# Optimization experiments

Measured on AMD Instinct MI355X. Metric: run time of the kernel, lower is better.

## Reference

```python
import jax, jax.numpy as jnp
import numpy as np

K_PRESERVED = 384   # num_preserved_tokens
NUM_HEADS = 6       # config.num_attention_heads // 2


def setup_inputs() -> dict:
    key = jax.random.key(0)
    ks = jax.random.split(key, 10)
    B, L, D, H = 16, 512, 768, 12
    U = D // 2  # num_units of the router attention
    s = 0.02
    return {
        "hidden_states": jax.random.normal(ks[0], (B, L, D), jnp.float32),
        "self_attention_scores": jax.random.uniform(ks[1], (B, H, L, L), jnp.float32),
        "Wq": jax.random.normal(ks[2], (D, U), jnp.float32) * s,
        "bq": jnp.zeros((U,), jnp.float32),
        "Wk": jax.random.normal(ks[3], (D, U), jnp.float32) * s,
        "bk": jnp.zeros((U,), jnp.float32),
        "Wv": jax.random.normal(ks[4], (D, U), jnp.float32) * s,
        "bv": jnp.zeros((U,), jnp.float32),
        "Wo": jax.random.normal(ks[5], (U, D), jnp.float32) * s,
        "bo": jnp.zeros((D,), jnp.float32),
    }


def _forward(hidden_states, self_attention_scores, Wq, bq, Wk, bk, Wv, bv, Wo, bo):
    B, L, D = hidden_states.shape
    K = K_PRESERVED
    r = L - K  # number of tokens merged away by ToMe
    batch_idx = jnp.arange(B)[:, None]

    class_token = hidden_states[:, :1, :]

    # importance = column sums of head-averaged attention with zeroed diagonal (detached)
    s = jax.lax.stop_gradient(jnp.mean(self_attention_scores, axis=1))  # [B,L,L]
    s = s * (1.0 - jnp.eye(L, dtype=s.dtype))
    importance = jnp.sum(s, axis=1)  # [B,L]
    _, important_idx = jax.lax.top_k(importance, K)  # [B,K]
    important_mask = jnp.zeros((B, L), bool).at[batch_idx, important_idx].set(True)

    # --- ToMe bipartite_soft_matching(hidden_states, r), mode='mean' ---
    metric = jax.lax.stop_gradient(hidden_states)
    metric = metric / jnp.linalg.norm(metric, axis=-1, keepdims=True)
    a, b = metric[:, ::2, :], metric[:, 1::2, :]            # [B,L/2,D] each
    sim = jnp.einsum('bid,bjd->bij', a, b)                   # [B,L/2,L/2]
    node_max = jnp.max(sim, axis=-1)                         # [B,L/2]
    node_idx = jnp.argmax(sim, axis=-1)                      # [B,L/2]
    edge_idx = jnp.argsort(-node_max, axis=-1)               # descending
    src_idx = edge_idx[:, :r]                                # merged src tokens
    unm_idx = edge_idx[:, r:]                                # unmerged src tokens
    dst_idx = jnp.take_along_axis(node_idx, src_idx, axis=1)  # [B,r]

    src_x = hidden_states[:, ::2, :]
    dst_x = hidden_states[:, 1::2, :]                        # [B,L/2,D]
    unm = jnp.take_along_axis(src_x, unm_idx[..., None], axis=1)   # [B,L/2-r,D]
    src_sel = jnp.take_along_axis(src_x, src_idx[..., None], axis=1)  # [B,r,D]
    # scatter_reduce(mean, include_self=True): (dst + sum srcs) / (1 + count)
    sums = dst_x.at[batch_idx, dst_idx].add(src_sel)
    counts = jnp.ones((B, L // 2), dst_x.dtype).at[batch_idx, dst_idx].add(1.0)
    dst_merged = sums / counts[..., None]
    preserved_tokens = jnp.concatenate([unm, dst_merged], axis=1)  # [B,K,D]

    # attention_mask is None -> sentences is the first token
    sentences = hidden_states[:, :1, :]

    # unpreserved tokens: boolean-mask gather, preserving original order
    order = jnp.argsort(important_mask.astype(jnp.int32), axis=1, stable=True)
    unp_idx = order[:, : L - K]                              # [B,L-K]
    unpreserved = hidden_states[batch_idx, unp_idx]          # [B,L-K,D]

    # router multi-head attention: query=sentence, key/value=unpreserved
    U = Wq.shape[1]
    hd = U // NUM_HEADS
    q = (sentences @ Wq + bq).reshape(B, 1, NUM_HEADS, hd)
    k = (unpreserved @ Wk + bk).reshape(B, L - K, NUM_HEADS, hd)
    v = (unpreserved @ Wv + bv).reshape(B, L - K, NUM_HEADS, hd)
    att = jax.nn.softmax(jnp.einsum('bqhd,bkhd->bhqk', q, k) / jnp.sqrt(jnp.asarray(hd, q.dtype)), axis=-1)
    ctx = jnp.einsum('bhqk,bkhd->bqhd', att, v).reshape(B, 1, U)
    new_token = ctx @ Wo + bo                                # [B,1,D]

    final_token = jnp.concatenate([class_token, preserved_tokens, new_token], axis=1)  # [B,K+2,D]
    return final_token


def reference(hidden_states, self_attention_scores, Wq, bq, Wk, bk, Wv, bv, Wo, bo):
    return _forward(hidden_states, self_attention_scores, Wq, bq, Wk, bk, Wv, bv, Wo, bo)
```

## Files before the change

kernel.cpp:

```cpp
#include <hip/hip_runtime.h>

#define BB 16
#define LL 512
#define DD 768
#define NHEAD 12
#define HALF 256
#define KPRES 384
#define RCNT 128
#define UDIM 384
#define NH2 6
#define HD 64

__device__ float              g_colsum_part[BB * NHEAD * 4 * LL];
__device__ unsigned long long g_nodep_part[BB * HALF * 4];
__device__ int g_unm[BB * RCNT];
__device__ int g_srctok[BB * RCNT];
__device__ int g_srcdst[BB * RCNT];
__device__ int g_unp[BB * RCNT];
__device__ float g_q[BB * UDIM];
__device__ float g_w2[BB * NH2 * DD];
__device__ float g_qbk[BB * NH2];
__device__ float g_ctx[BB * UDIM];

__global__ void k_main(const float* __restrict__ sc, const float* __restrict__ hs,
                       const float* __restrict__ Wq, const float* __restrict__ bq) {
    __shared__ __align__(16) float As[64][20];
    __shared__ __align__(16) float BsT[16][68];
    __shared__ float nA[64], nB[64];
    __shared__ unsigned long long cand[64][16];
    __shared__ float red[256];
    __shared__ __align__(16) float4 smc[256];
    __shared__ float h0q[DD];
    int blk = blockIdx.x;
    int t = threadIdx.x;

    if (blk >= 1024) {
        int qb = blk - 1024;
        int b = qb / NH2, h = qb % NH2;
        const float* hb = hs + (size_t)b * LL * DD;
        for (int d = t; d < DD; d += 256) h0q[d] = hb[d];
        __syncthreads();
        int u = t & 63, part = t >> 6;
        float a = 0.f;
        for (int d = part * 192; d < part * 192 + 192; d++)
            a += h0q[d] * Wq[(size_t)d * UDIM + h * HD + u];
        red[t] = a;
        __syncthreads();
        if (t < HD)
            g_q[b * UDIM + h * HD + t] =
                bq[h * HD + t] + red[t] + red[t + 64] + red[t + 128] + red[t + 192];
        return;
    }

    if (blk >= 256) {
        int cb = blk - 256;
        int ic = cb & 3;
        int bh = cb >> 2;
        const float* base = sc + (size_t)bh * LL * LL;
        int i0 = ic * 128;
        int p = t >> 7;
        int s = t & 127;
        float4 acc = {0.f, 0.f, 0.f, 0.f};
#pragma unroll 8
        for (int i = 0; i < 64; i++) {
            float4 v = ((const float4*)(base + (size_t)(i0 + 2 * i + p) * LL))[s];
            acc.x += v.x; acc.y += v.y; acc.z += v.z; acc.w += v.w;
        }
#pragma unroll
        for (int c = 0; c < 4; c++) {
            int cj = 4 * s + c;
            if (cj >= i0 && cj < i0 + 128 && (cj & 1) == p) {
                float d = base[(size_t)cj * LL + cj];
                if (c == 0) acc.x -= d; else if (c == 1) acc.y -= d;
                else if (c == 2) acc.z -= d; else acc.w -= d;
            }
        }
        smc[t] = acc;
        __syncthreads();
        if (t < 128) {
            float4 e = smc[t], o = smc[t + 128];
            float4 r;
            r.x = e.x + o.x; r.y = e.y + o.y; r.z = e.z + o.z; r.w = e.w + o.w;
            ((float4*)(g_colsum_part + (size_t)cb * LL))[t] = r;
        }
        return;
    }

    int b = blk >> 4, it = (blk >> 2) & 3, jt = blk & 3;
    int i0 = it * 64, j0 = jt * 64;
    const float* hb = hs + (size_t)b * LL * DD;
    {
        int rl = t >> 1, hf = t & 1;
        int grow = (rl < 64) ? 2 * (i0 + rl) : 2 * (j0 + rl - 64) + 1;
        const float4* rp = (const float4*)(hb + (size_t)grow * DD) + hf * 96;
        float4 ac = {0.f, 0.f, 0.f, 0.f};
#pragma unroll 4
        for (int q = 0; q < 96; q++) {
            float4 v = rp[q];
            ac.x += v.x * v.x; ac.y += v.y * v.y; ac.z += v.z * v.z; ac.w += v.w * v.w;
        }
        red[t] = (ac.x + ac.y) + (ac.z + ac.w);
        __syncthreads();
        if (t < 128) {
            float nrm = sqrtf(red[2 * t] + red[2 * t + 1]);
            if (t < 64) nA[t] = nrm; else nB[t - 64] = nrm;
        }
        __syncthreads();
    }
    int ti = t >> 4, tj = t & 15;
    float acc[4][4];
#pragma unroll
    for (int a = 0; a < 4; a++)
#pragma unroll
        for (int c = 0; c < 4; c++) acc[a][c] = 0.f;
    int sr = t >> 2, sc4 = t & 3;
    const float* arow = hb + (size_t)(2 * (i0 + sr)) * DD;
    const float* brow = hb + (size_t)(2 * (j0 + sr) + 1) * DD;
    float inA = nA[sr], inB = nB[sr];
    float4 a4 = ((const float4*)arow)[sc4];
    float4 b4 = ((const float4*)brow)[sc4];
    a4.x /= inA; a4.y /= inA; a4.z /= inA; a4.w /= inA;
    b4.x /= inB; b4.y /= inB; b4.z /= inB; b4.w /= inB;
    for (int s = 0; s < 48; s++) {
        __syncthreads();
        *(float4*)&As[sr][4 * sc4] = a4;
        BsT[4 * sc4 + 0][sr] = b4.x;
        BsT[4 * sc4 + 1][sr] = b4.y;
        BsT[4 * sc4 + 2][sr] = b4.z;
        BsT[4 * sc4 + 3][sr] = b4.w;
        __syncthreads();
        if (s + 1 < 48) {
            int d0 = (s + 1) * 16;
            a4 = ((const float4*)(arow + d0))[sc4];
            b4 = ((const float4*)(brow + d0))[sc4];
            a4.x /= inA; a4.y /= inA; a4.z /= inA; a4.w /= inA;
            b4.x /= inB; b4.y /= inB; b4.z /= inB; b4.w /= inB;
        }
#pragma unroll
        for (int c4 = 0; c4 < 4; c4++) {
            float4 av[4], bk4[4];
#pragma unroll
            for (int a = 0; a < 4; a++) av[a] = *(const float4*)&As[ti * 4 + a][4 * c4];
#pragma unroll
            for (int k = 0; k < 4; k++) bk4[k] = *(const float4*)&BsT[4 * c4 + k][4 * tj];
#pragma unroll
            for (int k = 0; k < 4; k++) {
#pragma unroll
                for (int a = 0; a < 4; a++) {
                    float ak = ((const float*)&av[a])[k];
#pragma unroll
                    for (int c = 0; c < 4; c++)
                        acc[a][c] += ak * ((const float*)&bk4[k])[c];
                }
            }
        }
    }
#pragma unroll
    for (int a = 0; a < 4; a++) {
        unsigned long long bp = 0ULL;
#pragma unroll
        for (int c = 0; c < 4; c++) {
            int jg = j0 + tj * 4 + c;
            unsigned u = __float_as_uint(acc[a][c]);
            u = (u & 0x80000000u) ? ~u : (u | 0x80000000u);
            unsigned long long pk = ((unsigned long long)u << 32) | (unsigned long long)(255 - jg);
            if (pk > bp) bp = pk;
        }
        cand[ti * 4 + a][tj] = bp;
    }
    __syncthreads();
    if (t < 64) {
        unsigned long long m = cand[t][0];
#pragma unroll
        for (int c2 = 1; c2 < 16; c2++) { unsigned long long v = cand[t][c2]; if (v > m) m = v; }
        g_nodep_part[((size_t)b * HALF + i0 + t) * 4 + jt] = m;
    }
}

__global__ void k_seledge(const float* __restrict__ Wk, const float* __restrict__ bk) {
    int blk = blockIdx.x, t = threadIdx.x;
    __shared__ float v[LL];
    __shared__ int pos[LL];
    __shared__ float nm[HALF];
    __shared__ int   ni[HALF];
    __shared__ __align__(16) float qsl[HD];

    if (blk >= BB) {
        int wb = blk - BB;
        int b = wb / NH2, h = wb % NH2;
        if (t < HD) qsl[t] = g_q[b * UDIM + h * HD + t];
        __syncthreads();
        if (t < 384) {
#pragma unroll
            for (int rep = 0; rep < 2; rep++) {
                int d = t + rep * 384;
                const float4* wrow = (const float4*)(Wk + (size_t)d * UDIM + h * HD);
                const float4* q4 = (const float4*)qsl;
                float4 s4 = {0.f, 0.f, 0.f, 0.f};
#pragma unroll
                for (int u4 = 0; u4 < 16; u4++) {
                    float4 w = wrow[u4], q = q4[u4];
                    s4.x += q.x * w.x; s4.y += q.y * w.y; s4.z += q.z * w.z; s4.w += q.w * w.w;
                }
                g_w2[((size_t)b * NH2 + h) * DD + d] = (s4.x + s4.y) + (s4.z + s4.w);
            }
        }
        if (t == 0) {
            float a = 0.f;
            for (int u = 0; u < HD; u++) a += qsl[u] * bk[h * HD + u];
            g_qbk[b * NH2 + h] = a;
        }
        return;
    }

    int b = blk;
    float imp = 0.f;
    for (int p = 0; p < NHEAD * 4; p++)
        imp += g_colsum_part[((size_t)b * NHEAD * 4 + p) * LL + t];
    v[t] = imp;
    __syncthreads();
    int cnt = 0;
    for (int k = 0; k < LL; k++) {
        float vk = v[k];
        cnt += (vk > imp) || (vk == imp && k < t);
    }
    int notp = (cnt >= KPRES) ? 1 : 0;
    pos[t] = notp;
    __syncthreads();
    for (int s = 1; s < LL; s <<= 1) {
        int add = (t >= s) ? pos[t - s] : 0;
        __syncthreads();
        pos[t] += add;
        __syncthreads();
    }
    if (notp) g_unp[b * RCNT + pos[t] - 1] = t;
    if (t < HALF) {
        unsigned long long p = g_nodep_part[((size_t)b * HALF + t) * 4 + 0];
#pragma unroll
        for (int q = 1; q < 4; q++) {
            unsigned long long w = g_nodep_part[((size_t)b * HALF + t) * 4 + q];
            if (w > p) p = w;
        }
        unsigned u = (unsigned)(p >> 32);
        unsigned bits = (u & 0x80000000u) ? (u & 0x7FFFFFFFu) : ~u;
        nm[t] = __uint_as_float(bits);
        ni[t] = 255 - (int)(p & 0xFFFFFFFFu);
    }
    __syncthreads();
    if (t < HALF) {
        float vv = nm[t];
        int cnt2 = 0;
        for (int k = 0; k < HALF; k++) {
            float vk = nm[k];
            cnt2 += (vk > vv) || (vk == vv && k < t);
        }
        if (cnt2 < RCNT) {
            g_srctok[b * RCNT + cnt2] = t;
            g_srcdst[b * RCNT + cnt2] = ni[t];
        } else {
            g_unm[b * RCNT + (cnt2 - RCNT)] = 2 * t;
        }
    }
}

__global__ void k_attn(const float* __restrict__ hs,
                       const float* __restrict__ Wv, const float* __restrict__ bv,
                       float* __restrict__ out) {
    int blk = blockIdx.x;
    int t = threadIdx.x;
    __shared__ __align__(16) float w2s[DD];
    __shared__ __align__(16) float hbars[DD];
    __shared__ int   toks[RCNT];
    __shared__ float att[RCNT];
    __shared__ float red[256];
    __shared__ float pm[4];
    __shared__ float qbkS;
    __shared__ int ss[RCNT], sd[RCNT];

    if (blk < BB * NH2) {
        int b = blk / NH2, h = blk % NH2;
        const float* hb = hs + (size_t)b * LL * DD;
        if (t < RCNT) toks[t] = g_unp[b * RCNT + t];
        for (int d = t; d < DD; d += 256) w2s[d] = g_w2[((size_t)b * NH2 + h) * DD + d];
        if (t == 0) qbkS = g_qbk[b * NH2 + h];
        __syncthreads();
        {
            int tok = t >> 1, half = t & 1;
            const float4* hr4 = (const float4*)(hb + (size_t)toks[tok] * DD) + half * 96;
            const float4* wk4 = (const float4*)w2s + half * 96;
            float4 s4 = {0.f, 0.f, 0.f, 0.f};
            for (int d4 = 0; d4 < 96; d4++) {
                float4 w = wk4[d4], x = hr4[d4];
                s4.x += w.x * x.x; s4.y += w.y * x.y; s4.z += w.z * x.z; s4.w += w.w * x.w;
            }
            red[t] = (s4.x + s4.y) + (s4.z + s4.w);
        }
        __syncthreads();
        float lg = -1e30f;
        if (t < RCNT) lg = (qbkS + red[2 * t] + red[2 * t + 1]) * 0.125f;
        float m = lg;
#pragma unroll
        for (int off = 32; off >= 1; off >>= 1) m = fmaxf(m, __shfl_xor(m, off, 64));
        if ((t & 63) == 0) pm[t >> 6] = m;
        __syncthreads();
        float mx = fmaxf(pm[0], pm[1]);
        float e = (t < RCNT) ? expf(lg - mx) : 0.f;
        float sume = e;
#pragma unroll
        for (int off = 32; off >= 1; off >>= 1) sume += __shfl_xor(sume, off, 64);
        __syncthreads();
        if ((t & 63) == 0) pm[t >> 6] = sume;
        __syncthreads();
        float inv = 1.f / (pm[0] + pm[1]);
        if (t < RCNT) att[t] = e * inv;
        __syncthreads();
        if (t < DD / 4) {
            float4 a = {0.f, 0.f, 0.f, 0.f};
            for (int s2 = 0; s2 < RCNT; s2++) {
                float4 x = ((const float4*)(hb + (size_t)toks[s2] * DD))[t];
                float w = att[s2];
                a.x += w * x.x; a.y += w * x.y; a.z += w * x.z; a.w += w * x.w;
            }
            *(float4*)&hbars[4 * t] = a;
        }
        __syncthreads();
        {
            int u = t & 63, part = t >> 6;
            float a = 0.f;
            for (int d = part * 192; d < part * 192 + 192; d++)
                a += hbars[d] * Wv[(size_t)d * UDIM + h * HD + u];
            red[t] = a;
            __syncthreads();
            if (t < HD)
                g_ctx[b * UDIM + h * HD + t] =
                    bv[h * HD + t] + red[t] + red[t + 64] + red[t + 128] + red[t + 192];
        }
        return;
    }

    int rblk = blk - BB * NH2;
    int row = rblk % 385, b = rblk / 385;
    float4* o4 = (float4*)(out + ((size_t)b * 386 + row) * DD);
    if (row == 0) {
        if (t < 192) {
            const float4* s4 = (const float4*)(hs + (size_t)b * LL * DD);
            o4[t] = s4[t];
        }
    } else if (row <= RCNT) {
        int tok = g_unm[b * RCNT + row - 1];
        if (t < 192) {
            const float4* s4 = (const float4*)(hs + ((size_t)b * LL + tok) * DD);
            o4[t] = s4[t];
        }
    } else {
        int j = row - 1 - RCNT;
        if (t < RCNT) { ss[t] = g_srctok[b * RCNT + t]; sd[t] = g_srcdst[b * RCNT + t]; }
        __syncthreads();
        if (t < 192) {
            float4 acc = ((const float4*)(hs + ((size_t)b * LL + 2 * j + 1) * DD))[t];
            float cnt = 1.f;
            for (int s2 = 0; s2 < RCNT; s2++) {
                if (sd[s2] == j) {
                    float4 v = ((const float4*)(hs + ((size_t)b * LL + 2 * ss[s2]) * DD))[t];
                    acc.x += v.x; acc.y += v.y; acc.z += v.z; acc.w += v.w;
                    cnt += 1.f;
                }
            }
            float4 r;
            r.x = acc.x / cnt; r.y = acc.y / cnt; r.z = acc.z / cnt; r.w = acc.w / cnt;
            o4[t] = r;
        }
    }
}

__global__ void k_newtok(const float* __restrict__ Wo, const float* __restrict__ bo,
                         float* __restrict__ out) {
    int b = blockIdx.x >> 2, q = blockIdx.x & 3;
    int t = threadIdx.x;
    __shared__ float c[UDIM];
    c[t] = g_ctx[b * UDIM + t];
    c[t + 192] = g_ctx[b * UDIM + t + 192];
    __syncthreads();
    int dd = q * 192 + t;
    float acc = bo[dd];
    for (int u = 0; u < UDIM; u++)
        acc += c[u] * Wo[(size_t)u * DD + dd];
    out[((size_t)b * 386 + 385) * DD + dd] = acc;
}

extern "C" void kernel_launch(void* const* d_in, const int* in_sizes, int n_in,
                              void* d_out, int out_size, void* d_ws, size_t ws_size,
                              hipStream_t stream) {
    const float* hs = (const float*)d_in[0];
    const float* sc = (const float*)d_in[1];
    const float* Wq = (const float*)d_in[2];
    const float* bq = (const float*)d_in[3];
    const float* Wk = (const float*)d_in[4];
    const float* bk = (const float*)d_in[5];
    const float* Wv = (const float*)d_in[6];
    const float* bv = (const float*)d_in[7];
    const float* Wo = (const float*)d_in[8];
    const float* bo = (const float*)d_in[9];
    float* out = (float*)d_out;
    (void)d_ws; (void)ws_size;

    k_main<<<256 + BB * NHEAD * 4 + BB * NH2, 256, 0, stream>>>(sc, hs, Wq, bq);
    k_seledge<<<BB + BB * NH2, 512, 0, stream>>>(Wk, bk);
    k_attn<<<BB * NH2 + BB * 385, 256, 0, stream>>>(hs, Wv, bv, out);
    k_newtok<<<BB * 4, 192, 0, stream>>>(Wo, bo, out);
}
```

Baseline: 451.4 us.

## Double-buffer the similarity GEMM tiles with a deeper K-step and a shared LDS union

Rewrites the bipartite-similarity tile loop to use a K-step of 32 instead of 16, with two shared-memory buffers so the next tile is written while the current one is computed. This halves the outer iterations and leaves one barrier per step instead of two, and global loads run two steps ahead. All per-branch shared arrays are merged into a single byte buffer with manual offsets, which keeps the larger double buffers from raising the LDS footprint. In exchange register pressure rises from holding four prefetched float4s, and the cand array now aliases the tile buffer after the final barrier.

Result: faster. 442.3 us (-2.0%).

```diff
diff --git a/kernel.cpp b/kernel.cpp
--- a/kernel.cpp
+++ b/kernel.cpp
@@ -22,19 +22,22 @@
 __device__ float g_qbk[BB * NH2];
 __device__ float g_ctx[BB * UDIM];
 
+#define OFF_AS   0
+#define OFF_BS   18432
+#define OFF_NA   35840
+#define OFF_NB   36096
+#define OFF_RED  36352
+#define SMEM_SZ  37376
+
 __global__ void k_main(const float* __restrict__ sc, const float* __restrict__ hs,
                        const float* __restrict__ Wq, const float* __restrict__ bq) {
-    __shared__ __align__(16) float As[64][20];
-    __shared__ __align__(16) float BsT[16][68];
-    __shared__ float nA[64], nB[64];
-    __shared__ unsigned long long cand[64][16];
-    __shared__ float red[256];
-    __shared__ __align__(16) float4 smc[256];
-    __shared__ float h0q[DD];
+    __shared__ __align__(16) char smem[SMEM_SZ];
     int blk = blockIdx.x;
     int t = threadIdx.x;
 
     if (blk >= 1024) {
+        float* h0q = (float*)smem;
+        float* red = (float*)(smem + OFF_RED);
         int qb = blk - 1024;
         int b = qb / NH2, h = qb % NH2;
         const float* hb = hs + (size_t)b * LL * DD;
@@ -53,6 +56,7 @@
     }
 
     if (blk >= 256) {
+        float4* smc = (float4*)smem;
         int cb = blk - 256;
         int ic = cb & 3;
         int bh = cb >> 2;
@@ -86,6 +90,13 @@
         return;
     }
 
+    float* AsF = (float*)smem;
+    float* BsF = (float*)(smem + OFF_BS);
+    float* nAp = (float*)(smem + OFF_NA);
+    float* nBp = (float*)(smem + OFF_NB);
+    float* red = (float*)(smem + OFF_RED);
+    unsigned long long* cand = (unsigned long long*)smem;
+
     int b = blk >> 4, it = (blk >> 2) & 3, jt = blk & 3;
     int i0 = it * 64, j0 = jt * 64;
     const float* hb = hs + (size_t)b * LL * DD;
@@ -103,7 +114,7 @@
         __syncthreads();
         if (t < 128) {
             float nrm = sqrtf(red[2 * t] + red[2 * t + 1]);
-            if (t < 64) nA[t] = nrm; else nB[t - 64] = nrm;
+            if (t < 64) nAp[t] = nrm; else nBp[t - 64] = nrm;
         }
         __syncthreads();
     }
@@ -113,36 +124,56 @@
     for (int a = 0; a < 4; a++)
 #pragma unroll
         for (int c = 0; c < 4; c++) acc[a][c] = 0.f;
-    int sr = t >> 2, sc4 = t & 3;
-    const float* arow = hb + (size_t)(2 * (i0 + sr)) * DD;
-    const float* brow = hb + (size_t)(2 * (j0 + sr) + 1) * DD;
-    float inA = nA[sr], inB = nB[sr];
-    float4 a4 = ((const float4*)arow)[sc4];
-    float4 b4 = ((const float4*)brow)[sc4];
-    a4.x /= inA; a4.y /= inA; a4.z /= inA; a4.w /= inA;
-    b4.x /= inB; b4.y /= inB; b4.z /= inB; b4.w /= inB;
-    for (int s = 0; s < 48; s++) {
-        __syncthreads();
-        *(float4*)&As[sr][4 * sc4] = a4;
-        BsT[4 * sc4 + 0][sr] = b4.x;
-        BsT[4 * sc4 + 1][sr] = b4.y;
-        BsT[4 * sc4 + 2][sr] = b4.z;
-        BsT[4 * sc4 + 3][sr] = b4.w;
-        __syncthreads();
-        if (s + 1 < 48) {
-            int d0 = (s + 1) * 16;
-            a4 = ((const float4*)(arow + d0))[sc4];
-            b4 = ((const float4*)(brow + d0))[sc4];
-            a4.x /= inA; a4.y /= inA; a4.z /= inA; a4.w /= inA;
-            b4.x /= inB; b4.y /= inB; b4.z /= inB; b4.w /= inB;
-        }
-#pragma unroll
-        for (int c4 = 0; c4 < 4; c4++) {
+    int r0 = t >> 3, sl = t & 7;
+    const float* arow0 = hb + (size_t)(2 * (i0 + r0)) * DD;
+    const float* arow1 = hb + (size_t)(2 * (i0 + r0 + 32)) * DD;
+    const float* brow0 = hb + (size_t)(2 * (j0 + r0) + 1) * DD;
+    const float* brow1 = hb + (size_t)(2 * (j0 + r0 + 32) + 1) * DD;
+    float inA0 = nAp[r0], inA1 = nAp[r0 + 32];
+    float inB0 = nBp[r0], inB1 = nBp[r0 + 32];
+    float4 pa0, pa1, pb0, pb1;
+#define LOADDIV(S)                                                              \
+    do {                                                                        \
+        int idx = 8 * (S) + sl;                                                 \
+        pa0 = ((const float4*)arow0)[idx];                                      \
+        pa1 = ((const float4*)arow1)[idx];                                      \
+        pb0 = ((const float4*)brow0)[idx];                                      \
+        pb1 = ((const float4*)brow1)[idx];                                      \
+        pa0.x /= inA0; pa0.y /= inA0; pa0.z /= inA0; pa0.w /= inA0;             \
+        pa1.x /= inA1; pa1.y /= inA1; pa1.z /= inA1; pa1.w /= inA1;             \
+        pb0.x /= inB0; pb0.y /= inB0; pb0.z /= inB0; pb0.w /= inB0;             \
+        pb1.x /= inB1; pb1.y /= inB1; pb1.z /= inB1; pb1.w /= inB1;             \
+    } while (0)
+#define WRITETILE(BUF)                                                          \
+    do {                                                                        \
+        *(float4*)&AsF[((BUF) * 64 + r0) * 36 + 4 * sl] = pa0;                  \
+        *(float4*)&AsF[((BUF) * 64 + r0 + 32) * 36 + 4 * sl] = pa1;             \
+        BsF[((BUF) * 32 + 4 * sl + 0) * 68 + r0] = pb0.x;                       \
+        BsF[((BUF) * 32 + 4 * sl + 1) * 68 + r0] = pb0.y;                       \
+        BsF[((BUF) * 32 + 4 * sl + 2) * 68 + r0] = pb0.z;                       \
+        BsF[((BUF) * 32 + 4 * sl + 3) * 68 + r0] = pb0.w;                       \
+        BsF[((BUF) * 32 + 4 * sl + 0) * 68 + r0 + 32] = pb1.x;                  \
+        BsF[((BUF) * 32 + 4 * sl + 1) * 68 + r0 + 32] = pb1.y;                  \
+        BsF[((BUF) * 32 + 4 * sl + 2) * 68 + r0 + 32] = pb1.z;                  \
+        BsF[((BUF) * 32 + 4 * sl + 3) * 68 + r0 + 32] = pb1.w;                  \
+    } while (0)
+    LOADDIV(0);
+    WRITETILE(0);
+    LOADDIV(1);
+    __syncthreads();
+    for (int s = 0; s < 24; s++) {
+        int cur = s & 1;
+        if (s + 1 < 24) WRITETILE(cur ^ 1);
+        if (s + 2 < 24) LOADDIV(s + 2);
+#pragma unroll
+        for (int c4 = 0; c4 < 8; c4++) {
             float4 av[4], bk4[4];
 #pragma unroll
-            for (int a = 0; a < 4; a++) av[a] = *(const float4*)&As[ti * 4 + a][4 * c4];
-#pragma unroll
-            for (int k = 0; k < 4; k++) bk4[k] = *(const float4*)&BsT[4 * c4 + k][4 * tj];
+            for (int a = 0; a < 4; a++)
+                av[a] = *(const float4*)&AsF[(cur * 64 + ti * 4 + a) * 36 + 4 * c4];
+#pragma unroll
+            for (int k = 0; k < 4; k++)
+                bk4[k] = *(const float4*)&BsF[(cur * 32 + 4 * c4 + k) * 68 + 4 * tj];
 #pragma unroll
             for (int k = 0; k < 4; k++) {
 #pragma unroll
@@ -154,6 +185,7 @@
                 }
             }
         }
+        __syncthreads();
     }
 #pragma unroll
     for (int a = 0; a < 4; a++) {
@@ -166,15 +198,17 @@
             unsigned long long pk = ((unsigned long long)u << 32) | (unsigned long long)(255 - jg);
             if (pk > bp) bp = pk;
         }
-        cand[ti * 4 + a][tj] = bp;
+        cand[(ti * 4 + a) * 16 + tj] = bp;
     }
     __syncthreads();
     if (t < 64) {
-        unsigned long long m = cand[t][0];
-#pragma unroll
-        for (int c2 = 1; c2 < 16; c2++) { unsigned long long v = cand[t][c2]; if (v > m) m = v; }
+        unsigned long long m = cand[t * 16];
+#pragma unroll
+        for (int c2 = 1; c2 < 16; c2++) { unsigned long long v = cand[t * 16 + c2]; if (v > m) m = v; }
         g_nodep_part[((size_t)b * HALF + i0 + t) * 4 + jt] = m;
     }
+#undef LOADDIV
+#undef WRITETILE
 }
 
 __global__ void k_seledge(const float* __restrict__ Wk, const float* __restrict__ bk) {
```
